# Optimization experiments

Hardware: AMD Instinct MI355X
Metric: run time of the kernel (lower is better)

## Reference

```python
import jax, jax.numpy as jnp
import numpy as np

B, IN, H, O, T = 4096, 128, 1024, 64, 25  # batch, static feat, hidden, outputs, steps


def setup_inputs() -> dict:
    key = jax.random.key(0)
    ks = jax.random.split(key, 11)
    s = 1.0 / np.sqrt(H)  # PyTorch LSTM/Linear uniform init scale
    u = lambda k, sh: jax.random.uniform(k, sh, jnp.float32, -s, s)
    return {
        "static_input": jax.random.normal(ks[0], (B, IN), jnp.float32),
        "W_ih0": u(ks[1], (4 * H, IN + O)),
        "W_hh0": u(ks[2], (4 * H, H)),
        "b_ih0": u(ks[3], (4 * H,)),
        "b_hh0": u(ks[4], (4 * H,)),
        "W_ih1": u(ks[5], (4 * H, H)),
        "W_hh1": u(ks[6], (4 * H, H)),
        "b_ih1": u(ks[7], (4 * H,)),
        "b_hh1": u(ks[8], (4 * H,)),
        "W_out": u(ks[9], (O, H)),
        "b_out": u(ks[10], (O,)),
        "num_steps": T,
    }


def _lstm_cell(x, h, c, W_ih, W_hh, b):
    # PyTorch gate order: input, forget, cell(g), output
    g = x @ W_ih.T + h @ W_hh.T + b
    i, f, gg, o = jnp.split(g, 4, axis=-1)
    c_new = jax.nn.sigmoid(f) * c + jax.nn.sigmoid(i) * jnp.tanh(gg)
    h_new = jax.nn.sigmoid(o) * jnp.tanh(c_new)
    return h_new, c_new


def reference(static_input, W_ih0, W_hh0, b_ih0, b_hh0,
              W_ih1, W_hh1, b_ih1, b_hh1, W_out, b_out, num_steps):
    b0 = b_ih0 + b_hh0
    b1 = b_ih1 + b_hh1
    batch = static_input.shape[0]
    hid = W_hh0.shape[1]
    out_dim = W_out.shape[0]
    z = jnp.zeros((batch, hid), jnp.float32)
    y0 = jnp.zeros((batch, out_dim), jnp.float32)  # output_seq[:, 0] is zeros at t=0

    def step(carry, _):
        h1, c1, h2, c2, y_prev = carry
        x = jnp.concatenate([static_input, y_prev], axis=-1)  # [B, IN+O]
        h1, c1 = _lstm_cell(x, h1, c1, W_ih0, W_hh0, b0)
        h2, c2 = _lstm_cell(h1, h2, c2, W_ih1, W_hh1, b1)
        y = h2 @ W_out.T + b_out  # [B, O]
        return (h1, c1, h2, c2, y), y

    _, ys = jax.lax.scan(step, (z, z, z, z, y0), None, length=num_steps)
    return jnp.transpose(ys, (1, 0, 2))  # [B, T, O]
```

## Files before the change

### kernel.cpp

```cpp
#include <hip/hip_runtime.h>

#define BATCH  4096
#define HID    1024
#define NOUT   64
#define TSTEPS 25
#define KA2    1280
#define KA2R   1216
#define KB     2048
#define LDY    1600

typedef __attribute__((ext_vector_type(8))) __bf16 bf16x8;
typedef __attribute__((ext_vector_type(4))) float  floatx4;

__device__ __forceinline__ unsigned short f2bf(float f) {
    union { float f; unsigned u; } v; v.f = f;
    unsigned r = v.u + 0x7fffu + ((v.u >> 16) & 1u);
    return (unsigned short)(r >> 16);
}
__device__ __forceinline__ float rcpf(float x) { return __builtin_amdgcn_rcpf(x); }
__device__ __forceinline__ float sigmf(float x) { return rcpf(1.0f + __expf(-x)); }
__device__ __forceinline__ float tanh_fast(float x) {
    float ax = fabsf(x);
    float e  = __expf(-2.0f * ax);
    float t  = (1.0f - e) * rcpf(1.0f + e);
    return copysignf(t, x);
}

#define GLDS16(gp, lp) __builtin_amdgcn_global_load_lds( \
    (const __attribute__((address_space(1))) void*)(gp), \
    (__attribute__((address_space(3))) void*)(lp), 16, 0, 0)

__global__ __launch_bounds__(512, 2) void lstm_gate_gemm(
    const unsigned short* __restrict__ X, int K,
    const unsigned short* __restrict__ W,
    const float* __restrict__ ginit,
    float* __restrict__ cell,
    unsigned short* __restrict__ d1, int ld1, int off1,
    unsigned short* __restrict__ d2, int ld2, int off2,
    float* __restrict__ dfp)
{
    __shared__ __align__(16) char smem[131072];

    const int tid  = threadIdx.x;
    const int lane = tid & 63;
    const int w    = tid >> 6;
    const int ql   = lane >> 4;
    const int lr   = lane & 15;
    const int wr   = w >> 2;
    const int wc   = w & 3;

    const int id  = blockIdx.y * 16 + blockIdx.x;
    const int xcd = id & 7;
    const int c   = id >> 3;
    const int bx  = (xcd & 3) * 4 + (c & 3);
    const int by  = (xcd >> 2) * 8 + (c >> 2);
    const int m0  = bx * 256;
    const int j0  = by * 64;

    const int s0  = w * 128 + lane;
    const int r0  = s0 >> 3;
    const int kc0 = (s0 & 7) ^ (r0 & 7);
    const unsigned sOff = (unsigned)s0 * 16;
    const unsigned short* sA[2];
    const unsigned short* sB[2];
    sA[0] = X + (size_t)(m0 + r0) * K + kc0 * 8;
    sA[1] = X + (size_t)(m0 + 128 + r0) * K + kc0 * 8;
    {
        const int nb0 = r0, nb1 = 128 + r0;
        sB[0] = W + (size_t)((nb0 & 3) * HID + j0 + (nb0 >> 2)) * K + kc0 * 8;
        sB[1] = W + (size_t)((nb1 & 3) * HID + j0 + (nb1 >> 2)) * K + kc0 * 8;
    }

#define STAGE_A(h, tt, p) do { \
    const unsigned short* _s = sA[h] + (size_t)(tt) * 64; \
    char* _d = smem + (p) + (h) * 16384 + sOff; \
    GLDS16(_s, _d); \
    GLDS16(_s + 8 * (size_t)K, _d + 1024); \
} while (0)

#define STAGE_B(h, tt, p) do { \
    const unsigned short* _s = sB[h] + (size_t)(tt) * 64; \
    char* _d = smem + (p) + 32768 + (h) * 16384 + sOff; \
    GLDS16(_s, _d); \
    GLDS16(_s + 2 * (size_t)K, _d + 1024); \
} while (0)

    unsigned offA[4], offB[2];
#pragma unroll
    for (int fi = 0; fi < 4; ++fi) {
        int r = wr * 64 + fi * 16 + lr;
        offA[fi] = (unsigned)((r * 8 + (ql ^ (r & 7))) * 16);
    }
#pragma unroll
    for (int fj = 0; fj < 2; ++fj) {
        int r = wc * 32 + fj * 16 + lr;
        offB[fj] = (unsigned)(32768 + (r * 8 + (ql ^ (r & 7))) * 16);
    }

#define LOAD_A(AV, BASE) do { \
    const char* _ab = smem + (BASE); \
    _Pragma("unroll") \
    for (int fi = 0; fi < 4; ++fi) { \
        AV[fi][0] = *(const bf16x8*)(_ab + offA[fi]); \
        AV[fi][1] = *(const bf16x8*)(_ab + (offA[fi] ^ 64u)); \
    } \
} while (0)

#define LOAD_B(BV, BASE) do { \
    const char* _bb = smem + (BASE); \
    _Pragma("unroll") \
    for (int fj = 0; fj < 2; ++fj) { \
        BV[fj][0] = *(const bf16x8*)(_bb + offB[fj]); \
        BV[fj][1] = *(const bf16x8*)(_bb + (offB[fj] ^ 64u)); \
    } \
} while (0)

#define MFMA16(Q, AV, BV) do { \
    __builtin_amdgcn_s_setprio(1); \
    _Pragma("unroll") \
    for (int fi = 0; fi < 4; ++fi) \
    _Pragma("unroll") \
    for (int fj = 0; fj < 2; ++fj) \
    _Pragma("unroll") \
    for (int kk = 0; kk < 2; ++kk) \
        acc[Q][fi][fj] = __builtin_amdgcn_mfma_f32_16x16x32_bf16( \
            AV[fi][kk], BV[fj][kk], acc[Q][fi][fj], 0, 0, 0); \
    __builtin_amdgcn_s_setprio(0); \
} while (0)

    floatx4 acc[4][4][2];
#pragma unroll
    for (int q = 0; q < 4; ++q)
#pragma unroll
        for (int i = 0; i < 4; ++i)
#pragma unroll
            for (int j = 0; j < 2; ++j)
                acc[q][i][j] = floatx4{0.f, 0.f, 0.f, 0.f};

    const int NT = K >> 6;

    bf16x8 av0[4][2], av1[4][2], bv0[2][2], bv1[2][2];

    STAGE_A(0, 0, 0); STAGE_B(0, 0, 0); STAGE_A(1, 0, 0); STAGE_B(1, 0, 0);
    STAGE_B(0, 1, 65536); STAGE_A(1, 1, 65536);
    asm volatile("s_waitcnt vmcnt(4)");
    __builtin_amdgcn_s_barrier();
    __builtin_amdgcn_sched_barrier(0);
    LOAD_A(av0, 0);
    LOAD_B(bv0, 0);
    LOAD_B(bv1, 16384);
    __builtin_amdgcn_sched_barrier(0);

    int par = 0;
    for (int t = 0; t < NT; ++t) {
        const int cur = par << 16;
        const int np  = cur ^ 65536;
        const int t1  = (t + 1 < NT) ? t + 1 : NT - 1;
        const int t2  = (t + 2 < NT) ? t + 2 : NT - 1;
        __builtin_amdgcn_s_barrier();
        __builtin_amdgcn_sched_barrier(0);
        LOAD_A(av1, cur + 16384);
        STAGE_A(0, t1, np);
        __builtin_amdgcn_sched_barrier(0);
        MFMA16(0, av0, bv0);
        __builtin_amdgcn_s_barrier();
        __builtin_amdgcn_sched_barrier(0);
        STAGE_B(1, t1, np);
        __builtin_amdgcn_sched_barrier(0);
        MFMA16(1, av0, bv1);
        asm volatile("s_waitcnt vmcnt(2)");
        __builtin_amdgcn_s_barrier();
        __builtin_amdgcn_sched_barrier(0);
        LOAD_A(av0, np);
        STAGE_B(0, t2, cur);
        __builtin_amdgcn_sched_barrier(0);
        MFMA16(2, av1, bv1);
        asm volatile("s_waitcnt vmcnt(2)");
        __builtin_amdgcn_s_barrier();
        __builtin_amdgcn_sched_barrier(0);
        LOAD_B(bv1, np + 16384);
        STAGE_A(1, t2, cur);
        __builtin_amdgcn_sched_barrier(0);
        MFMA16(3, av1, bv0);
        __builtin_amdgcn_sched_barrier(0);
        LOAD_B(bv0, np);
        par ^= 1;
    }

    asm volatile("s_waitcnt vmcnt(0)");
    __builtin_amdgcn_s_barrier();

    float* scratch = (float*)(void*)smem + w * 640;
    const int jj   = lane & 7;
    const int rsel = lane >> 3;

#pragma unroll
    for (int qd = 0; qd < 4; ++qd) {
        const int qa = (qd >= 2) ? 1 : 0;
        const int qb = (qd == 1 || qd == 2) ? 1 : 0;
        const int rowbase = m0 + qa * 128 + wr * 64;
        const int jg = j0 + qb * 32 + wc * 8 + jj;
        const float4 gi = *(const float4*)(ginit + (size_t)jg * 4);
#pragma unroll
        for (int fi = 0; fi < 4; ++fi) {
#pragma unroll
            for (int fj = 0; fj < 2; ++fj)
#pragma unroll
                for (int r = 0; r < 4; ++r)
                    scratch[(ql * 4 + r) * 36 + fj * 16 + lr] = acc[qd][fi][fj][r];
            asm volatile("" ::: "memory");
#pragma unroll
            for (int p = 0; p < 2; ++p) {
                const int row = rsel + p * 8;
                const float4 g = *(const float4*)(scratch + row * 36 + jj * 4);
                const int b = rowbase + fi * 16 + row;
                float iv = sigmf(g.x + gi.x);
                float fv = sigmf(g.y + gi.y);
                float gv = tanh_fast(g.z + gi.z);
                float ov = sigmf(g.w + gi.w);
                size_t ci = (size_t)b * HID + jg;
                float cn = fv * cell[ci] + iv * gv;
                cell[ci] = cn;
                float hv = ov * tanh_fast(cn);
                unsigned short hb = f2bf(hv);
                d1[(size_t)b * ld1 + off1 + jg] = hb;
                if (d2)  d2[(size_t)b * ld2 + off2 + jg] = hb;
                if (dfp) dfp[(size_t)b * HID + jg] = hv;
            }
            asm volatile("" ::: "memory");
        }
    }
#undef MFMA16
#undef LOAD_A
#undef LOAD_B
#undef STAGE_A
#undef STAGE_B
}

__global__ __launch_bounds__(256) void out_gemm(
    const float* __restrict__ h2, const float* __restrict__ wt,
    const float* __restrict__ bout, float* __restrict__ y,
    unsigned short* __restrict__ xn)
{
    __shared__ float hl[8 * 1024];
    const int tid = threadIdx.x;
    const int b0 = blockIdx.x * 8;
#pragma unroll
    for (int r = 0; r < 8; ++r) {
        int f4 = r * 256 + tid;
        *(float4*)(hl + f4 * 4) = *(const float4*)(h2 + (size_t)b0 * 1024 + f4 * 4);
    }
    __syncthreads();
    const int o  = tid & 63;
    const int wv = tid >> 6;
    float acc0 = 0.f, acc1 = 0.f;
#pragma unroll 8
    for (int k = 0; k < 1024; ++k) {
        float wvv = wt[k * 64 + o];
        acc0 += hl[(wv * 2 + 0) * 1024 + k] * wvv;
        acc1 += hl[(wv * 2 + 1) * 1024 + k] * wvv;
    }
    float bo = bout[o];
    int b = b0 + wv * 2;
    float y0 = acc0 + bo, y1 = acc1 + bo;
    y[(size_t)b * LDY + o] = y0;
    y[(size_t)(b + 1) * LDY + o] = y1;
    xn[(size_t)b * KA2 + o] = f2bf(y0);
    xn[(size_t)(b + 1) * KA2 + o] = f2bf(y1);
}

__global__ void build_woutT(const float* __restrict__ wout, float* __restrict__ wt)
{
    int idx = blockIdx.x * 256 + threadIdx.x;
    int o = idx & 63, k = idx >> 6;
    wt[idx] = wout[(size_t)o * 1024 + k];
}

__global__ void build_bias(const float* __restrict__ a, const float* __restrict__ b,
                           float* __restrict__ o)
{
    int idx = blockIdx.x * 256 + threadIdx.x;
    int gate = idx & 3, j = idx >> 2;
    int n = gate * 1024 + j;
    o[idx] = a[n] + b[n];
}

__global__ __launch_bounds__(256) void build_w0(
    const float* __restrict__ wih, const float* __restrict__ whh,
    unsigned short* __restrict__ w0)
{
    int idx = blockIdx.x * 256 + threadIdx.x;
    int n = idx / 320;
    int c = (idx - n * 320) * 4;
    float4 v = {0.f, 0.f, 0.f, 0.f};
    if (c < 64)        v = *(const float4*)(wih + (size_t)n * 192 + 128 + c);
    else if (c < 192)  v = *(const float4*)(wih + (size_t)n * 192 + (c - 64));
    else if (c < 1216) v = *(const float4*)(whh + (size_t)n * 1024 + (c - 192));
    ushort4 o;
    o.x = f2bf(v.x); o.y = f2bf(v.y); o.z = f2bf(v.z); o.w = f2bf(v.w);
    *(ushort4*)(w0 + (size_t)n * KA2 + c) = o;
}

__global__ __launch_bounds__(256) void build_w1(
    const float* __restrict__ wih, const float* __restrict__ whh,
    unsigned short* __restrict__ w1)
{
    int idx = blockIdx.x * 256 + threadIdx.x;
    int n = idx >> 9;
    int c = (idx & 511) * 4;
    float4 v;
    if (c < 1024) v = *(const float4*)(wih + (size_t)n * 1024 + c);
    else          v = *(const float4*)(whh + (size_t)n * 1024 + (c - 1024));
    ushort4 o;
    o.x = f2bf(v.x); o.y = f2bf(v.y); o.z = f2bf(v.z); o.w = f2bf(v.w);
    *(ushort4*)(w1 + (size_t)n * KB + c) = o;
}

__global__ __launch_bounds__(256) void build_x0static(
    const float* __restrict__ stat, unsigned short* __restrict__ xa,
    unsigned short* __restrict__ xb)
{
    int idx = blockIdx.x * 256 + threadIdx.x;
    int b = idx >> 5;
    int c = (idx & 31) * 4;
    float4 v = *(const float4*)(stat + (size_t)b * 128 + c);
    ushort4 o;
    o.x = f2bf(v.x); o.y = f2bf(v.y); o.z = f2bf(v.z); o.w = f2bf(v.w);
    *(ushort4*)(xa + (size_t)b * KA2 + 64 + c) = o;
    *(ushort4*)(xb + (size_t)b * KA2 + 64 + c) = o;
}

extern "C" void kernel_launch(void* const* d_in, const int* in_sizes, int n_in,
                              void* d_out, int out_size, void* d_ws, size_t ws_size,
                              hipStream_t stream)
{
    (void)in_sizes; (void)n_in; (void)out_size; (void)ws_size;
    const float* static_in = (const float*)d_in[0];
    const float* Wih0 = (const float*)d_in[1];
    const float* Whh0 = (const float*)d_in[2];
    const float* bih0 = (const float*)d_in[3];
    const float* bhh0 = (const float*)d_in[4];
    const float* Wih1 = (const float*)d_in[5];
    const float* Whh1 = (const float*)d_in[6];
    const float* bih1 = (const float*)d_in[7];
    const float* bhh1 = (const float*)d_in[8];
    const float* Wout = (const float*)d_in[9];
    const float* bout = (const float*)d_in[10];
    float* out = (float*)d_out;

    char* p = (char*)d_ws;
    size_t off = 0;
    auto take = [&](size_t n) { char* r = p + off; off += (n + 255) & ~(size_t)255; return r; };

    unsigned short* W0   = (unsigned short*)take((size_t)4096 * KA2 * 2);
    unsigned short* W1   = (unsigned short*)take((size_t)4096 * KB * 2);
    float*          B1b  = (float*)take(4096 * 4);
    float*          B0b  = (float*)take(4096 * 4);
    float*          WoT  = (float*)take((size_t)1024 * 64 * 4);
    float*          H2f  = (float*)take((size_t)BATCH * HID * 4);
    float*          C1   = (float*)take((size_t)BATCH * HID * 4);
    float*          C2   = (float*)take((size_t)BATCH * HID * 4);
    unsigned short* X0a  = (unsigned short*)take((size_t)BATCH * KA2 * 2);
    unsigned short* X0b  = (unsigned short*)take((size_t)BATCH * KA2 * 2);
    unsigned short* X1a  = (unsigned short*)take((size_t)BATCH * KB * 2);
    unsigned short* X1b  = (unsigned short*)take((size_t)BATCH * KB * 2);

    hipMemsetAsync(C1, 0, (size_t)BATCH * HID * 4, stream);
    hipMemsetAsync(C2, 0, (size_t)BATCH * HID * 4, stream);
    hipMemsetAsync(X0a, 0, (size_t)BATCH * KA2 * 2, stream);
    hipMemsetAsync(X0b, 0, (size_t)BATCH * KA2 * 2, stream);
    hipMemsetAsync(X1a, 0, (size_t)BATCH * KB * 2, stream);

    build_w0<<<5120, 256, 0, stream>>>(Wih0, Whh0, W0);
    build_w1<<<8192, 256, 0, stream>>>(Wih1, Whh1, W1);
    build_woutT<<<256, 256, 0, stream>>>(Wout, WoT);
    build_bias<<<16, 256, 0, stream>>>(bih0, bhh0, B0b);
    build_bias<<<16, 256, 0, stream>>>(bih1, bhh1, B1b);
    build_x0static<<<512, 256, 0, stream>>>(static_in, X0a, X0b);

    dim3 grid(16, 16);
    for (int t = 0; t < TSTEPS; ++t) {
        unsigned short* X0c = (t & 1) ? X0b : X0a;
        unsigned short* X0n = (t & 1) ? X0a : X0b;
        unsigned short* X1c = (t & 1) ? X1b : X1a;
        unsigned short* X1n = (t & 1) ? X1a : X1b;
        lstm_gate_gemm<<<grid, 512, 0, stream>>>(X0c, KA2, W0, B0b, C1,
                                                 X1c, KB, 0, X0n, KA2, 192, nullptr);
        lstm_gate_gemm<<<grid, 512, 0, stream>>>(X1c, KB, W1, B1b, C2,
                                                 X1n, KB, 1024, nullptr, 0, 0, H2f);
        out_gemm<<<512, 256, 0, stream>>>(H2f, WoT, bout, out + t * NOUT, X0n);
    }
}
```

Before: 3.939 ms.

## Deepen GEMM prefetch, interleave MFMA with loads, prefetch cell state, widen out_gemm

The gate GEMM main loop now prefetches both LDS buffers two K-tiles ahead instead of one. It splits each MFMA block so that one fragment row issues before the LDS reads and global-to-LDS staging, with the rest after, to overlap memory traffic with matrix math. The epilogue loads all previous cell-state values into registers before the activation loop so global loads are not serialized behind LDS scratch traffic, at the cost of extra registers. The output GEMM processes 16 batch rows per block with 4 accumulators per thread, halving the grid and reusing each weight load across more rows.

```diff
diff --git a/kernel.cpp b/kernel.cpp
--- a/kernel.cpp
+++ b/kernel.cpp
@@ -29,6 +29,8 @@
 #define GLDS16(gp, lp) __builtin_amdgcn_global_load_lds( \
     (const __attribute__((address_space(1))) void*)(gp), \
     (__attribute__((address_space(3))) void*)(lp), 16, 0, 0)
+
+#define SB() __builtin_amdgcn_sched_barrier(0)
 
 __global__ __launch_bounds__(512, 2) void lstm_gate_gemm(
     const unsigned short* __restrict__ X, int K,
@@ -115,10 +117,10 @@
     } \
 } while (0)
 
-#define MFMA16(Q, AV, BV) do { \
+#define MFMA_PART(Q, AV, BV, F0, F1) do { \
     __builtin_amdgcn_s_setprio(1); \
     _Pragma("unroll") \
-    for (int fi = 0; fi < 4; ++fi) \
+    for (int fi = (F0); fi < (F1); ++fi) \
     _Pragma("unroll") \
     for (int fj = 0; fj < 2; ++fj) \
     _Pragma("unroll") \
@@ -141,48 +143,58 @@
 
     bf16x8 av0[4][2], av1[4][2], bv0[2][2], bv1[2][2];
 
-    STAGE_A(0, 0, 0); STAGE_B(0, 0, 0); STAGE_A(1, 0, 0); STAGE_B(1, 0, 0);
-    STAGE_B(0, 1, 65536); STAGE_A(1, 1, 65536);
-    asm volatile("s_waitcnt vmcnt(4)");
+    STAGE_B(1, 0, 0); STAGE_A(1, 0, 0); STAGE_A(0, 0, 0); STAGE_B(0, 0, 0);
+    STAGE_B(1, 1, 65536); STAGE_A(1, 1, 65536); STAGE_A(0, 1, 65536); STAGE_B(0, 1, 65536);
+    asm volatile("s_waitcnt vmcnt(8)");
     __builtin_amdgcn_s_barrier();
-    __builtin_amdgcn_sched_barrier(0);
+    SB();
     LOAD_A(av0, 0);
     LOAD_B(bv0, 0);
     LOAD_B(bv1, 16384);
-    __builtin_amdgcn_sched_barrier(0);
+    SB();
 
     int par = 0;
     for (int t = 0; t < NT; ++t) {
         const int cur = par << 16;
         const int np  = cur ^ 65536;
-        const int t1  = (t + 1 < NT) ? t + 1 : NT - 1;
         const int t2  = (t + 2 < NT) ? t + 2 : NT - 1;
         __builtin_amdgcn_s_barrier();
-        __builtin_amdgcn_sched_barrier(0);
+        SB();
+        MFMA_PART(0, av0, bv0, 0, 1);
+        SB();
         LOAD_A(av1, cur + 16384);
-        STAGE_A(0, t1, np);
-        __builtin_amdgcn_sched_barrier(0);
-        MFMA16(0, av0, bv0);
+        STAGE_B(1, t2, cur);
+        SB();
+        MFMA_PART(0, av0, bv0, 1, 4);
+        SB();
         __builtin_amdgcn_s_barrier();
-        __builtin_amdgcn_sched_barrier(0);
-        STAGE_B(1, t1, np);
-        __builtin_amdgcn_sched_barrier(0);
-        MFMA16(1, av0, bv1);
-        asm volatile("s_waitcnt vmcnt(2)");
+        SB();
+        MFMA_PART(1, av0, bv1, 0, 1);
+        SB();
+        STAGE_A(1, t2, cur);
+        SB();
+        MFMA_PART(1, av0, bv1, 1, 4);
+        SB();
+        asm volatile("s_waitcnt vmcnt(6)");
         __builtin_amdgcn_s_barrier();
-        __builtin_amdgcn_sched_barrier(0);
+        SB();
+        MFMA_PART(2, av1, bv1, 0, 1);
+        SB();
         LOAD_A(av0, np);
+        STAGE_A(0, t2, cur);
+        SB();
+        MFMA_PART(2, av1, bv1, 1, 4);
+        SB();
+        asm volatile("s_waitcnt vmcnt(6)");
+        __builtin_amdgcn_s_barrier();
+        SB();
+        MFMA_PART(3, av1, bv0, 0, 1);
+        SB();
+        LOAD_B(bv1, np + 16384);
         STAGE_B(0, t2, cur);
-        __builtin_amdgcn_sched_barrier(0);
-        MFMA16(2, av1, bv1);
-        asm volatile("s_waitcnt vmcnt(2)");
-        __builtin_amdgcn_s_barrier();
-        __builtin_amdgcn_sched_barrier(0);
-        LOAD_B(bv1, np + 16384);
-        STAGE_A(1, t2, cur);
-        __builtin_amdgcn_sched_barrier(0);
-        MFMA16(3, av1, bv0);
-        __builtin_amdgcn_sched_barrier(0);
+        SB();
+        MFMA_PART(3, av1, bv0, 1, 4);
+        SB();
         LOAD_B(bv0, np);
         par ^= 1;
     }
@@ -194,13 +206,29 @@
     const int jj   = lane & 7;
     const int rsel = lane >> 3;
 
+    float  cpre[4][4][2];
+    float4 gi4[4];
 #pragma unroll
     for (int qd = 0; qd < 4; ++qd) {
         const int qa = (qd >= 2) ? 1 : 0;
         const int qb = (qd == 1 || qd == 2) ? 1 : 0;
         const int rowbase = m0 + qa * 128 + wr * 64;
         const int jg = j0 + qb * 32 + wc * 8 + jj;
-        const float4 gi = *(const float4*)(ginit + (size_t)jg * 4);
+        gi4[qd] = *(const float4*)(ginit + (size_t)jg * 4);
+#pragma unroll
+        for (int fi = 0; fi < 4; ++fi)
+#pragma unroll
+            for (int p = 0; p < 2; ++p)
+                cpre[qd][fi][p] = cell[(size_t)(rowbase + fi * 16 + rsel + p * 8) * HID + jg];
+    }
+
+#pragma unroll
+    for (int qd = 0; qd < 4; ++qd) {
+        const int qa = (qd >= 2) ? 1 : 0;
+        const int qb = (qd == 1 || qd == 2) ? 1 : 0;
+        const int rowbase = m0 + qa * 128 + wr * 64;
+        const int jg = j0 + qb * 32 + wc * 8 + jj;
+        const float4 gi = gi4[qd];
 #pragma unroll
         for (int fi = 0; fi < 4; ++fi) {
 #pragma unroll
@@ -219,7 +247,7 @@
                 float gv = tanh_fast(g.z + gi.z);
                 float ov = sigmf(g.w + gi.w);
                 size_t ci = (size_t)b * HID + jg;
-                float cn = fv * cell[ci] + iv * gv;
+                float cn = fv * cpre[qd][fi][p] + iv * gv;
                 cell[ci] = cn;
                 float hv = ov * tanh_fast(cn);
                 unsigned short hb = f2bf(hv);
@@ -230,7 +258,7 @@
             asm volatile("" ::: "memory");
         }
     }
-#undef MFMA16
+#undef MFMA_PART
 #undef LOAD_A
 #undef LOAD_B
 #undef STAGE_A
@@ -242,31 +270,35 @@
     const float* __restrict__ bout, float* __restrict__ y,
     unsigned short* __restrict__ xn)
 {
-    __shared__ float hl[8 * 1024];
+    __shared__ float hl[16 * 1024];
     const int tid = threadIdx.x;
-    const int b0 = blockIdx.x * 8;
-#pragma unroll
-    for (int r = 0; r < 8; ++r) {
+    const int b0 = blockIdx.x * 16;
+#pragma unroll
+    for (int r = 0; r < 16; ++r) {
         int f4 = r * 256 + tid;
         *(float4*)(hl + f4 * 4) = *(const float4*)(h2 + (size_t)b0 * 1024 + f4 * 4);
     }
     __syncthreads();
     const int o  = tid & 63;
     const int wv = tid >> 6;
-    float acc0 = 0.f, acc1 = 0.f;
+    float a0 = 0.f, a1 = 0.f, a2 = 0.f, a3 = 0.f;
 #pragma unroll 8
     for (int k = 0; k < 1024; ++k) {
         float wvv = wt[k * 64 + o];
-        acc0 += hl[(wv * 2 + 0) * 1024 + k] * wvv;
-        acc1 += hl[(wv * 2 + 1) * 1024 + k] * wvv;
+        const float* hr = hl + (wv * 4) * 1024 + k;
+        a0 += hr[0]    * wvv;
+        a1 += hr[1024] * wvv;
+        a2 += hr[2048] * wvv;
+        a3 += hr[3072] * wvv;
     }
     float bo = bout[o];
-    int b = b0 + wv * 2;
-    float y0 = acc0 + bo, y1 = acc1 + bo;
-    y[(size_t)b * LDY + o] = y0;
-    y[(size_t)(b + 1) * LDY + o] = y1;
-    xn[(size_t)b * KA2 + o] = f2bf(y0);
-    xn[(size_t)(b + 1) * KA2 + o] = f2bf(y1);
+    int b = b0 + wv * 4;
+    float yv[4] = {a0 + bo, a1 + bo, a2 + bo, a3 + bo};
+#pragma unroll
+    for (int r = 0; r < 4; ++r) {
+        y[(size_t)(b + r) * LDY + o] = yv[r];
+        xn[(size_t)(b + r) * KA2 + o] = f2bf(yv[r]);
+    }
 }
 
 __global__ void build_woutT(const float* __restrict__ wout, float* __restrict__ wt)
@@ -388,6 +420,6 @@
                                                  X1c, KB, 0, X0n, KA2, 192, nullptr);
         lstm_gate_gemm<<<grid, 512, 0, stream>>>(X1c, KB, W1, B1b, C2,
                                                  X1n, KB, 1024, nullptr, 0, 0, H2f);
-        out_gemm<<<512, 256, 0, stream>>>(H2f, WoT, bout, out + t * NOUT, X0n);
-    }
-}
+        out_gemm<<<256, 256, 0, stream>>>(H2f, WoT, bout, out + t * NOUT, X0n);
+    }
+}
```

Result: faster. 3.655 ms (-7.2%).
